# Performance work log

Hardware: AMD Instinct MI355X
Metric: run time of the kernel (lower is better)

Reference implementation:

```python
import jax, jax.numpy as jnp
import numpy as np

B, N_CTX, NY, NX = 8, 1024, 128, 128
DIM_Y = 2
DOMAIN = 10.0


def setup_inputs() -> dict:
    key = jax.random.key(0)
    k1, k2 = jax.random.split(key)
    X_c = jax.random.uniform(k1, (B, N_CTX, 2), dtype=jnp.float32) * DOMAIN
    Y_c = jax.random.normal(k2, (B, N_CTX, DIM_Y), dtype=jnp.float32)
    ys = jnp.linspace(0.0, DOMAIN, NY, dtype=jnp.float32)
    xs = jnp.linspace(0.0, DOMAIN, NX, dtype=jnp.float32)
    gy, gx = jnp.meshgrid(ys, xs, indexing='ij')  # [NY,NX]
    grid = jnp.stack([gx, gy], axis=-1).reshape(-1, 2)  # [NY*NX, 2]
    log_l_scale = jnp.zeros((1,), dtype=jnp.float32)  # log(1.0)
    return {"X_c": X_c, "Y_c": Y_c, "grid": grid, "log_l_scale": log_l_scale}


def reference(X_c, Y_c, grid, log_l_scale):
    # l_scale = exp(clamp(log_l_scale, -5, 5))
    l = jnp.exp(jnp.clip(log_l_scale[0], -5.0, 5.0))
    # Pairwise squared distances grid-to-context: [B, G, N]
    diff = grid[None, :, None, :] - X_c[:, None, :, :]  # [B,G,N,2]
    d2 = jnp.sum(diff * diff, axis=-1)                  # [B,G,N]
    Gram = jnp.exp(-d2 / (2.0 * l * l))                 # RBF kernel
    # Expand Y with leading ones channel (density channel)
    ones = jnp.ones((B, N_CTX, 1), dtype=Y_c.dtype)
    Expand_Y = jnp.concatenate([ones, Y_c], axis=-1)    # [B,N,3]
    FM = jnp.einsum('bgn,bnc->bgc', Gram, Expand_Y)     # [B,G,3]
    density = FM[..., :1]
    feats = FM[..., 1:] / density                       # normalize by density
    FM = jnp.concatenate([density, feats], axis=-1)
    # reshape to image layout [B, C, NY, NX]
    return FM.reshape(B, NY, NX, DIM_Y + 1).transpose(0, 3, 1, 2)
```

## Files before the change

### kernel.cpp

```cpp
#include <hip/hip_runtime.h>


#define NCTX 1024
#define NG   128
#define NB   8
#define CH   128
#define LPAD 4
#define STRIDE (CH + LPAD)

__device__ __forceinline__ void ctx_step(float ex0, float ex1, float ex2, float ex3,
                                         float ey0, float ey1, float y1, float y2,
                                         float (&d)[8], float (&a)[8], float (&c)[8])
{
    const float exv[4] = {ex0, ex1, ex2, ex3};
    const float eyv[2] = {ey0, ey1};
    #pragma unroll
    for (int i = 0; i < 4; ++i) {
        #pragma unroll
        for (int j = 0; j < 2; ++j) {
            const float w = exv[i] * eyv[j];
            d[i * 2 + j] += w;
            a[i * 2 + j] = fmaf(w, y1, a[i * 2 + j]);
            c[i * 2 + j] = fmaf(w, y2, c[i * 2 + j]);
        }
    }
}

template<int NSPLIT>
__global__ __launch_bounds__(256, 3)
void eds_partial(const float* __restrict__ Xc,
                 const float* __restrict__ Yc,
                 const float* __restrict__ gridp,
                 const float* __restrict__ logl,
                 float* __restrict__ part)
{
    constexpr int SC = NCTX / NSPLIT;
    __shared__ float sEx[64][STRIDE];
    __shared__ float sEy[32][STRIDE];

    const int tid = threadIdx.x;
    const int ixl = tid & 15;
    const int iyl = tid >> 4;
    int blk = blockIdx.x;
    const int s = blk % NSPLIT; blk /= NSPLIT;
    const int tile = blk & 7;
    const int b    = blk >> 3;
    const int tx0 = (tile & 1) * 64;
    const int ty0 = (tile >> 1) * 32;

    const float ls = fminf(5.0f, fmaxf(-5.0f, logl[0]));
    const float l  = expf(ls);
    const float scale = -0.7213475204444817f / (l * l);

    float gx[4], gy[2];
    #pragma unroll
    for (int i = 0; i < 4; ++i) gx[i] = gridp[2 * (tx0 + ixl + 16 * i)];
    gy[0] = gridp[2 * ((ty0 + iyl) * NG) + 1];
    gy[1] = gridp[2 * ((ty0 + iyl + 16) * NG) + 1];

    float d[8], a[8], c[8];
    #pragma unroll
    for (int i = 0; i < 8; ++i) { d[i] = 0.0f; a[i] = 0.0f; c[i] = 0.0f; }

    for (int ch = 0; ch < SC / CH; ++ch) {
        const int cb = s * SC + ch * CH;
        __syncthreads();

        {
            const float* Xp = Xc + ((size_t)b * NCTX + cb + 8 * iyl) * 2;
            float xv[8];
            #pragma unroll
            for (int t = 0; t < 4; ++t) {
                const float4 p = ((const float4*)Xp)[t];
                xv[2 * t]     = p.x;
                xv[2 * t + 1] = p.z;
            }
            #pragma unroll
            for (int i = 0; i < 4; ++i) {
                float4 e0, e1; float dx;
                dx = gx[i] - xv[0]; e0.x = exp2f(dx * dx * scale);
                dx = gx[i] - xv[1]; e0.y = exp2f(dx * dx * scale);
                dx = gx[i] - xv[2]; e0.z = exp2f(dx * dx * scale);
                dx = gx[i] - xv[3]; e0.w = exp2f(dx * dx * scale);
                dx = gx[i] - xv[4]; e1.x = exp2f(dx * dx * scale);
                dx = gx[i] - xv[5]; e1.y = exp2f(dx * dx * scale);
                dx = gx[i] - xv[6]; e1.z = exp2f(dx * dx * scale);
                dx = gx[i] - xv[7]; e1.w = exp2f(dx * dx * scale);
                *(float4*)&sEx[ixl + 16 * i][8 * iyl]     = e0;
                *(float4*)&sEx[ixl + 16 * i][8 * iyl + 4] = e1;
            }
        }
        {
            const float* Xq = Xc + ((size_t)b * NCTX + cb + 8 * ixl) * 2;
            float yv[8];
            #pragma unroll
            for (int t = 0; t < 4; ++t) {
                const float4 p = ((const float4*)Xq)[t];
                yv[2 * t]     = p.y;
                yv[2 * t + 1] = p.w;
            }
            #pragma unroll
            for (int j = 0; j < 2; ++j) {
                float4 e0, e1; float dy;
                dy = gy[j] - yv[0]; e0.x = exp2f(dy * dy * scale);
                dy = gy[j] - yv[1]; e0.y = exp2f(dy * dy * scale);
                dy = gy[j] - yv[2]; e0.z = exp2f(dy * dy * scale);
                dy = gy[j] - yv[3]; e0.w = exp2f(dy * dy * scale);
                dy = gy[j] - yv[4]; e1.x = exp2f(dy * dy * scale);
                dy = gy[j] - yv[5]; e1.y = exp2f(dy * dy * scale);
                dy = gy[j] - yv[6]; e1.z = exp2f(dy * dy * scale);
                dy = gy[j] - yv[7]; e1.w = exp2f(dy * dy * scale);
                *(float4*)&sEy[iyl + 16 * j][8 * ixl]     = e0;
                *(float4*)&sEy[iyl + 16 * j][8 * ixl + 4] = e1;
            }
        }
        __syncthreads();

        const float4* yp = (const float4*)(Yc + ((size_t)b * NCTX + cb) * 2);

        #pragma unroll 4
        for (int k = 0; k < CH / 4; ++k) {
            const float4 ex0 = *(const float4*)&sEx[ixl     ][4 * k];
            const float4 ex1 = *(const float4*)&sEx[ixl + 16][4 * k];
            const float4 ex2 = *(const float4*)&sEx[ixl + 32][4 * k];
            const float4 ex3 = *(const float4*)&sEx[ixl + 48][4 * k];
            const float4 ey0 = *(const float4*)&sEy[iyl     ][4 * k];
            const float4 ey1 = *(const float4*)&sEy[iyl + 16][4 * k];
            const float4 ya = yp[2 * k];
            const float4 yb = yp[2 * k + 1];
            ctx_step(ex0.x, ex1.x, ex2.x, ex3.x, ey0.x, ey1.x, ya.x, ya.y, d, a, c);
            ctx_step(ex0.y, ex1.y, ex2.y, ex3.y, ey0.y, ey1.y, ya.z, ya.w, d, a, c);
            ctx_step(ex0.z, ex1.z, ex2.z, ex3.z, ey0.z, ey1.z, yb.x, yb.y, d, a, c);
            ctx_step(ex0.w, ex1.w, ex2.w, ex3.w, ey0.w, ey1.w, yb.z, yb.w, d, a, c);
        }
    }

    const size_t G = (size_t)NG * NG;
    float* P = part + ((size_t)(s * NB + b) * 3) * G;
    #pragma unroll
    for (int i = 0; i < 4; ++i) {
        #pragma unroll
        for (int j = 0; j < 2; ++j) {
            const int o = (ty0 + iyl + 16 * j) * NG + (tx0 + ixl + 16 * i);
            P[        o] = d[i * 2 + j];
            P[G     + o] = a[i * 2 + j];
            P[2 * G + o] = c[i * 2 + j];
        }
    }
}

template<int NSPLIT>
__global__ __launch_bounds__(256)
void eds_combine(const float* __restrict__ part, float* __restrict__ out)
{
    const size_t G = (size_t)NG * NG;
    const int t = blockIdx.x * 256 + threadIdx.x;
    const int b = t >> 14;
    const int o = t & (NG * NG - 1);
    float d = 0.0f, a1 = 0.0f, a2 = 0.0f;
    #pragma unroll
    for (int s = 0; s < NSPLIT; ++s) {
        const float* P = part + ((size_t)(s * NB + b) * 3) * G;
        d  += P[o];
        a1 += P[G + o];
        a2 += P[2 * G + o];
    }
    out[((size_t)b * 3 + 0) * G + o] = d;
    out[((size_t)b * 3 + 1) * G + o] = a1 / d;
    out[((size_t)b * 3 + 2) * G + o] = a2 / d;
}

extern "C" void kernel_launch(void* const* d_in, const int* in_sizes, int n_in,
                              void* d_out, int out_size, void* d_ws, size_t ws_size,
                              hipStream_t stream) {
    const float* Xc = (const float*)d_in[0];
    const float* Yc = (const float*)d_in[1];
    const float* gr = (const float*)d_in[2];
    const float* ll = (const float*)d_in[3];
    float* out  = (float*)d_out;
    float* part = (float*)d_ws;

    const size_t need8 = (size_t)8 * NB * 3 * NG * NG * sizeof(float);
    if (ws_size >= need8) {
        eds_partial<8><<<dim3(NB * 8 * 8), dim3(256), 0, stream>>>(Xc, Yc, gr, ll, part);
        eds_combine<8><<<dim3(NB * NG * NG / 256), dim3(256), 0, stream>>>(part, out);
    } else {
        eds_partial<1><<<dim3(NB * 8), dim3(256), 0, stream>>>(Xc, Yc, gr, ll, part);
        eds_combine<1><<<dim3(NB * NG * NG / 256), dim3(256), 0, stream>>>(part, out);
    }
}
```

Baseline: 81.87 us.

## Enlarge per-thread grid tile to 4x4 and vectorize the split-K combine

The partial kernel now computes a 64x64 grid tile per block, with a 4x4 output tile per thread instead of 4x2. Separable exp factors are staged in shared memory in 64-context chunks, with each wave computing both x and y factors. The context split rises from 8 to 16, and the combine kernel is vectorized to float4 loads and stores. The aim is more FMA work per shared-memory load and cheaper combining, at the cost of higher register pressure (occupancy hint drops to 2) and twice the partial-buffer traffic.

Result: slower. 87.52 us (+6.9%).

```diff
diff --git a/kernel.cpp b/kernel.cpp
--- a/kernel.cpp
+++ b/kernel.cpp
@@ -4,30 +4,11 @@
 #define NCTX 1024
 #define NG   128
 #define NB   8
-#define CH   128
-#define LPAD 4
-#define STRIDE (CH + LPAD)
-
-__device__ __forceinline__ void ctx_step(float ex0, float ex1, float ex2, float ex3,
-                                         float ey0, float ey1, float y1, float y2,
-                                         float (&d)[8], float (&a)[8], float (&c)[8])
-{
-    const float exv[4] = {ex0, ex1, ex2, ex3};
-    const float eyv[2] = {ey0, ey1};
-    #pragma unroll
-    for (int i = 0; i < 4; ++i) {
-        #pragma unroll
-        for (int j = 0; j < 2; ++j) {
-            const float w = exv[i] * eyv[j];
-            d[i * 2 + j] += w;
-            a[i * 2 + j] = fmaf(w, y1, a[i * 2 + j]);
-            c[i * 2 + j] = fmaf(w, y2, c[i * 2 + j]);
-        }
-    }
-}
+#define CH   64
+#define STR  66
 
 template<int NSPLIT>
-__global__ __launch_bounds__(256, 3)
+__global__ __launch_bounds__(256, 2)
 void eds_partial(const float* __restrict__ Xc,
                  const float* __restrict__ Yc,
                  const float* __restrict__ gridp,
@@ -35,103 +16,87 @@
                  float* __restrict__ part)
 {
     constexpr int SC = NCTX / NSPLIT;
-    __shared__ float sEx[64][STRIDE];
-    __shared__ float sEy[32][STRIDE];
+    __shared__ float sEx[64 * STR];
+    __shared__ float sEy[64 * STR];
 
-    const int tid = threadIdx.x;
-    const int ixl = tid & 15;
-    const int iyl = tid >> 4;
+    const int tid  = threadIdx.x;
+    const int ixl  = tid & 15;
+    const int iyl  = tid >> 4;
+    const int lane = tid & 63;
+    const int wv   = tid >> 6;
+
     int blk = blockIdx.x;
-    const int s = blk % NSPLIT; blk /= NSPLIT;
-    const int tile = blk & 7;
-    const int b    = blk >> 3;
+    const int s    = blk % NSPLIT;  blk /= NSPLIT;
+    const int tile = blk & 3;
+    const int b    = blk >> 2;
     const int tx0 = (tile & 1) * 64;
-    const int ty0 = (tile >> 1) * 32;
+    const int ty0 = (tile >> 1) * 64;
 
     const float ls = fminf(5.0f, fmaxf(-5.0f, logl[0]));
     const float l  = expf(ls);
     const float scale = -0.7213475204444817f / (l * l);
 
-    float gx[4], gy[2];
+    float d[16], a[16], c[16];
     #pragma unroll
-    for (int i = 0; i < 4; ++i) gx[i] = gridp[2 * (tx0 + ixl + 16 * i)];
-    gy[0] = gridp[2 * ((ty0 + iyl) * NG) + 1];
-    gy[1] = gridp[2 * ((ty0 + iyl + 16) * NG) + 1];
-
-    float d[8], a[8], c[8];
-    #pragma unroll
-    for (int i = 0; i < 8; ++i) { d[i] = 0.0f; a[i] = 0.0f; c[i] = 0.0f; }
+    for (int i = 0; i < 16; ++i) { d[i] = 0.0f; a[i] = 0.0f; c[i] = 0.0f; }
 
     for (int ch = 0; ch < SC / CH; ++ch) {
         const int cb = s * SC + ch * CH;
-        __syncthreads();
+        if (ch) __syncthreads();
 
         {
-            const float* Xp = Xc + ((size_t)b * NCTX + cb + 8 * iyl) * 2;
-            float xv[8];
+            const float gxr = gridp[2 * (tx0 + lane)];
+            const float gyr = gridp[2 * ((ty0 + lane) * NG) + 1];
+            const float* Xp = Xc + ((size_t)b * NCTX + cb + 16 * wv) * 2;
+            float xv[16], yv[16];
+            #pragma unroll
+            for (int t = 0; t < 8; ++t) {
+                const float4 p = ((const float4*)Xp)[t];
+                xv[2 * t]     = p.x;  yv[2 * t]     = p.y;
+                xv[2 * t + 1] = p.z;  yv[2 * t + 1] = p.w;
+            }
+            float ex[16], ey[16];
+            #pragma unroll
+            for (int t = 0; t < 16; ++t) {
+                const float dx = gxr - xv[t];
+                const float dy = gyr - yv[t];
+                ex[t] = exp2f(dx * dx * scale);
+                ey[t] = exp2f(dy * dy * scale);
+            }
             #pragma unroll
             for (int t = 0; t < 4; ++t) {
-                const float4 p = ((const float4*)Xp)[t];
-                xv[2 * t]     = p.x;
-                xv[2 * t + 1] = p.z;
-            }
-            #pragma unroll
-            for (int i = 0; i < 4; ++i) {
-                float4 e0, e1; float dx;
-                dx = gx[i] - xv[0]; e0.x = exp2f(dx * dx * scale);
-                dx = gx[i] - xv[1]; e0.y = exp2f(dx * dx * scale);
-                dx = gx[i] - xv[2]; e0.z = exp2f(dx * dx * scale);
-                dx = gx[i] - xv[3]; e0.w = exp2f(dx * dx * scale);
-                dx = gx[i] - xv[4]; e1.x = exp2f(dx * dx * scale);
-                dx = gx[i] - xv[5]; e1.y = exp2f(dx * dx * scale);
-                dx = gx[i] - xv[6]; e1.z = exp2f(dx * dx * scale);
-                dx = gx[i] - xv[7]; e1.w = exp2f(dx * dx * scale);
-                *(float4*)&sEx[ixl + 16 * i][8 * iyl]     = e0;
-                *(float4*)&sEx[ixl + 16 * i][8 * iyl + 4] = e1;
-            }
-        }
-        {
-            const float* Xq = Xc + ((size_t)b * NCTX + cb + 8 * ixl) * 2;
-            float yv[8];
-            #pragma unroll
-            for (int t = 0; t < 4; ++t) {
-                const float4 p = ((const float4*)Xq)[t];
-                yv[2 * t]     = p.y;
-                yv[2 * t + 1] = p.w;
-            }
-            #pragma unroll
-            for (int j = 0; j < 2; ++j) {
-                float4 e0, e1; float dy;
-                dy = gy[j] - yv[0]; e0.x = exp2f(dy * dy * scale);
-                dy = gy[j] - yv[1]; e0.y = exp2f(dy * dy * scale);
-                dy = gy[j] - yv[2]; e0.z = exp2f(dy * dy * scale);
-                dy = gy[j] - yv[3]; e0.w = exp2f(dy * dy * scale);
-                dy = gy[j] - yv[4]; e1.x = exp2f(dy * dy * scale);
-                dy = gy[j] - yv[5]; e1.y = exp2f(dy * dy * scale);
-                dy = gy[j] - yv[6]; e1.z = exp2f(dy * dy * scale);
-                dy = gy[j] - yv[7]; e1.w = exp2f(dy * dy * scale);
-                *(float4*)&sEy[iyl + 16 * j][8 * ixl]     = e0;
-                *(float4*)&sEy[iyl + 16 * j][8 * ixl + 4] = e1;
+                *(float4*)&sEx[lane * STR + 16 * wv + 4 * t] =
+                    make_float4(ex[4*t], ex[4*t+1], ex[4*t+2], ex[4*t+3]);
+                *(float4*)&sEy[lane * STR + 16 * wv + 4 * t] =
+                    make_float4(ey[4*t], ey[4*t+1], ey[4*t+2], ey[4*t+3]);
             }
         }
         __syncthreads();
 
         const float4* yp = (const float4*)(Yc + ((size_t)b * NCTX + cb) * 2);
+        const float* exb = &sEx[ixl * STR];
+        const float* eyb = &sEy[iyl * STR];
 
         #pragma unroll 4
-        for (int k = 0; k < CH / 4; ++k) {
-            const float4 ex0 = *(const float4*)&sEx[ixl     ][4 * k];
-            const float4 ex1 = *(const float4*)&sEx[ixl + 16][4 * k];
-            const float4 ex2 = *(const float4*)&sEx[ixl + 32][4 * k];
-            const float4 ex3 = *(const float4*)&sEx[ixl + 48][4 * k];
-            const float4 ey0 = *(const float4*)&sEy[iyl     ][4 * k];
-            const float4 ey1 = *(const float4*)&sEy[iyl + 16][4 * k];
-            const float4 ya = yp[2 * k];
-            const float4 yb = yp[2 * k + 1];
-            ctx_step(ex0.x, ex1.x, ex2.x, ex3.x, ey0.x, ey1.x, ya.x, ya.y, d, a, c);
-            ctx_step(ex0.y, ex1.y, ex2.y, ex3.y, ey0.y, ey1.y, ya.z, ya.w, d, a, c);
-            ctx_step(ex0.z, ex1.z, ex2.z, ex3.z, ey0.z, ey1.z, yb.x, yb.y, d, a, c);
-            ctx_step(ex0.w, ex1.w, ex2.w, ex3.w, ey0.w, ey1.w, yb.z, yb.w, d, a, c);
+        for (int k = 0; k < CH / 2; ++k) {
+            float2 ex[4], ey[4];
+            #pragma unroll
+            for (int i = 0; i < 4; ++i) ex[i] = *(const float2*)&exb[16 * i * STR + 2 * k];
+            #pragma unroll
+            for (int j = 0; j < 4; ++j) ey[j] = *(const float2*)&eyb[16 * j * STR + 2 * k];
+            const float4 y = yp[k];
+            #pragma unroll
+            for (int i = 0; i < 4; ++i) {
+                #pragma unroll
+                for (int j = 0; j < 4; ++j) {
+                    const int o = i * 4 + j;
+                    float w;
+                    w = ex[i].x * ey[j].x;
+                    d[o] += w; a[o] = fmaf(w, y.x, a[o]); c[o] = fmaf(w, y.y, c[o]);
+                    w = ex[i].y * ey[j].y;
+                    d[o] += w; a[o] = fmaf(w, y.z, a[o]); c[o] = fmaf(w, y.w, c[o]);
+                }
+            }
         }
     }
 
@@ -140,11 +105,11 @@
     #pragma unroll
     for (int i = 0; i < 4; ++i) {
         #pragma unroll
-        for (int j = 0; j < 2; ++j) {
+        for (int j = 0; j < 4; ++j) {
             const int o = (ty0 + iyl + 16 * j) * NG + (tx0 + ixl + 16 * i);
-            P[        o] = d[i * 2 + j];
-            P[G     + o] = a[i * 2 + j];
-            P[2 * G + o] = c[i * 2 + j];
+            P[        o] = d[i * 4 + j];
+            P[G     + o] = a[i * 4 + j];
+            P[2 * G + o] = c[i * 4 + j];
         }
     }
 }
@@ -155,19 +120,24 @@
 {
     const size_t G = (size_t)NG * NG;
     const int t = blockIdx.x * 256 + threadIdx.x;
-    const int b = t >> 14;
-    const int o = t & (NG * NG - 1);
-    float d = 0.0f, a1 = 0.0f, a2 = 0.0f;
+    const int b = t >> 12;
+    const int o4 = t & 4095;
+    float4 d = make_float4(0.f, 0.f, 0.f, 0.f);
+    float4 a1 = d, a2 = d;
     #pragma unroll
     for (int s = 0; s < NSPLIT; ++s) {
-        const float* P = part + ((size_t)(s * NB + b) * 3) * G;
-        d  += P[o];
-        a1 += P[G + o];
-        a2 += P[2 * G + o];
+        const float4* P = (const float4*)(part + ((size_t)(s * NB + b) * 3) * G);
+        const float4 pd = P[o4];
+        const float4 p1 = P[G / 4 + o4];
+        const float4 p2 = P[G / 2 + o4];
+        d.x += pd.x; d.y += pd.y; d.z += pd.z; d.w += pd.w;
+        a1.x += p1.x; a1.y += p1.y; a1.z += p1.z; a1.w += p1.w;
+        a2.x += p2.x; a2.y += p2.y; a2.z += p2.z; a2.w += p2.w;
     }
-    out[((size_t)b * 3 + 0) * G + o] = d;
-    out[((size_t)b * 3 + 1) * G + o] = a1 / d;
-    out[((size_t)b * 3 + 2) * G + o] = a2 / d;
+    float4* O = (float4*)(out + (size_t)b * 3 * G);
+    O[o4] = d;
+    O[G / 4 + o4] = make_float4(a1.x / d.x, a1.y / d.y, a1.z / d.z, a1.w / d.w);
+    O[G / 2 + o4] = make_float4(a2.x / d.x, a2.y / d.y, a2.z / d.z, a2.w / d.w);
 }
 
 extern "C" void kernel_launch(void* const* d_in, const int* in_sizes, int n_in,
@@ -180,12 +150,12 @@
     float* out  = (float*)d_out;
     float* part = (float*)d_ws;
 
-    const size_t need8 = (size_t)8 * NB * 3 * NG * NG * sizeof(float);
-    if (ws_size >= need8) {
-        eds_partial<8><<<dim3(NB * 8 * 8), dim3(256), 0, stream>>>(Xc, Yc, gr, ll, part);
-        eds_combine<8><<<dim3(NB * NG * NG / 256), dim3(256), 0, stream>>>(part, out);
+    const size_t need16 = (size_t)16 * NB * 3 * NG * NG * sizeof(float);
+    if (ws_size >= need16) {
+        eds_partial<16><<<dim3(NB * 4 * 16), dim3(256), 0, stream>>>(Xc, Yc, gr, ll, part);
+        eds_combine<16><<<dim3(NB * NG * NG / 4 / 256), dim3(256), 0, stream>>>(part, out);
     } else {
-        eds_partial<1><<<dim3(NB * 8), dim3(256), 0, stream>>>(Xc, Yc, gr, ll, part);
-        eds_combine<1><<<dim3(NB * NG * NG / 256), dim3(256), 0, stream>>>(part, out);
+        eds_partial<4><<<dim3(NB * 4 * 4), dim3(256), 0, stream>>>(Xc, Yc, gr, ll, part);
+        eds_combine<4><<<dim3(NB * NG * NG / 4 / 256), dim3(256), 0, stream>>>(part, out);
     }
 }
```
